# Kernel tuning notes

Hardware: AMD Instinct MI355X
Metric: run time of the kernel (lower is better)

## Reference

```python
import jax, jax.numpy as jnp
import numpy as np
from jax import lax

L, BSZ, H, W, U, P = 16, 8, 32, 32, 128, 256
KB = KC = KD = 3
NUM_GROUPS = 32
DT_MIN, DT_MAX = 1e-3, 1e-1
EPS = 1e-5


def setup_inputs() -> dict:
    key = jax.random.key(0)
    ks = jax.random.split(key, 10)
    return {
        "input_sequence": jax.random.normal(ks[0], (L, BSZ, H, W, U), jnp.float32),
        "x0": jax.random.normal(ks[1], (BSZ, H, W, P), jnp.float32),
        # negative real parts of continuous-time eigenvalues
        "Lambda_re": -(0.5 * jax.random.uniform(ks[2], (P,), jnp.float32) + 1e-2),
        "Lambda_im": jax.random.normal(ks[3], (P,), jnp.float32) * jnp.pi,
        # B param (P,U,kB,kB,2) real/imag stacked (he-normal scale)
        "B_ri": jax.random.normal(ks[4], (P, U, KB, KB, 2), jnp.float32) / np.sqrt(U * KB * KB),
        # C param (U,P,kC,kC,2) real/imag stacked
        "C_ri": jax.random.normal(ks[5], (U, P, KC, KC, 2), jnp.float32) / np.sqrt(P * KC * KC),
        "log_step": jax.random.uniform(ks[6], (P,), jnp.float32) * (np.log(DT_MAX) - np.log(DT_MIN)) + np.log(DT_MIN),
        # diagonal (depthwise) feedthrough D conv kernel, HWIO with I=1
        "D_kernel": jax.random.normal(ks[7], (KD, KD, 1, U), jnp.float32) / KD,
        "gn_scale": jnp.ones((U,), jnp.float32),
        "gn_bias": jnp.zeros((U,), jnp.float32),
    }


def _conv(x, k):
    # x: (N,H,W,Cin), k: (kh,kw,Cin,Cout), SAME padding, stride 1
    return lax.conv_general_dilated(x, k, (1, 1), 'SAME',
                                    dimension_numbers=('NHWC', 'HWIO', 'NHWC'))


def _group_norm(x, scale, bias):
    n, h, w, c = x.shape
    xg = x.reshape(n, h, w, NUM_GROUPS, c // NUM_GROUPS)
    mu = xg.mean(axis=(1, 2, 4), keepdims=True)
    var = xg.var(axis=(1, 2, 4), keepdims=True)
    xg = (xg - mu) * lax.rsqrt(var + EPS)
    return xg.reshape(n, h, w, c) * scale + bias


def reference(input_sequence, x0, Lambda_re, Lambda_im, B_ri, C_ri, log_step,
              D_kernel, gn_scale, gn_bias):
    # ---- discretization (faithful to source discretize_zoh: A_bar = Lambda*Delta, B_bar = Delta*B_tilde) ----
    Lam = jnp.minimum(Lambda_re, -1e-4) + 1j * Lambda_im      # clip_eigs, (P,) complex64
    step = jnp.exp(log_step)                                   # (P,)
    A_bar = Lam * step                                         # (P,) complex64
    # B_bar = (1/Lambda)*Lambda_bar*B_tilde = Delta * B_tilde, laid out HWIO (kB,kB,U,P)
    Bk_r = jnp.transpose(B_ri[..., 0] * step[:, None, None, None], (2, 3, 1, 0))
    Bk_i = jnp.transpose(B_ri[..., 1] * step[:, None, None, None], (2, 3, 1, 0))
    # C_tilde kernel HWIO (kC,kC,P,U)
    Ck_r = jnp.transpose(C_ri[..., 0], (2, 3, 1, 0))
    Ck_i = jnp.transpose(C_ri[..., 1], (2, 3, 1, 0))

    # ---- B (*) u for all timesteps (fold L into batch) ----
    u = input_sequence.reshape(L * BSZ, H, W, U)
    Bus = (_conv(u, Bk_r) + 1j * _conv(u, Bk_i)).reshape(L, BSZ, H, W, P)  # complex64
    Bus = Bus.at[0].add(A_bar * x0.astype(Bus.dtype))

    # ---- diagonal parallel scan: x_k = A * x_{k-1} + (B (*) u_k) ----
    A_elems = jnp.broadcast_to(A_bar[None, None, None, None, :], (L, 1, 1, 1, P))

    def binop(qi, qj):
        Ai, bi = qi
        Aj, bj = qj
        return Aj * Ai, Aj * bi + bj

    _, xs = lax.associative_scan(binop, (A_elems, Bus))        # xs: (L,BSZ,H,W,P) complex

    # ---- ys = 2*Re(C (*) x) ----
    xr = xs.real.reshape(L * BSZ, H, W, P)
    xi = xs.imag.reshape(L * BSZ, H, W, P)
    ys = 2.0 * (_conv(xr, Ck_r) - _conv(xi, Ck_i))             # (L*BSZ,H,W,U)

    # ---- C_D conv head ('standard' Diag_CD_Conv): diagonal D feedthrough + GroupNorm + act ----
    Du = lax.conv_general_dilated(u, D_kernel, (1, 1), 'SAME',
                                  dimension_numbers=('NHWC', 'HWIO', 'NHWC'),
                                  feature_group_count=U)
    h = jax.nn.gelu(_group_norm(ys + Du, gn_scale, gn_bias))
    ys_out = h.reshape(L, BSZ, H, W, U)

    x_last = xs[-1]                                            # (BSZ,H,W,P) complex
    x_last_ri = jnp.stack([x_last.real, x_last.imag], axis=-1) # real view for harness
    return x_last_ri, ys_out
```

## Files before the change

### kernel.cpp

```cpp
#include <hip/hip_runtime.h>
#include <hip/hip_bf16.h>
#include <math.h>

#define Ldim 16
#define BATCH 8
#define HWdim 1024

typedef __attribute__((ext_vector_type(8))) short s8v;
typedef __attribute__((ext_vector_type(4))) short s4v;
typedef __attribute__((ext_vector_type(2))) short s2v;
typedef __attribute__((ext_vector_type(4))) float f32x4;
typedef __attribute__((ext_vector_type(2))) float f32x2;

__device__ __forceinline__ short f2bf(float f) {
    __hip_bfloat16 h = __float2bfloat16(f);
    return __builtin_bit_cast(short, h);
}
__device__ __forceinline__ float bf2f(short s) {
    __hip_bfloat16 h = __builtin_bit_cast(__hip_bfloat16, s);
    return __bfloat162float(h);
}

__device__ __forceinline__ void gload_lds16(const short* g, short* l) {
    __builtin_amdgcn_global_load_lds(
        (const __attribute__((address_space(1))) void*)g,
        (__attribute__((address_space(3))) void*)l, 16, 0, 0);
}

__global__ __launch_bounds__(256)
void prep_kernel(const float* __restrict__ Lre, const float* __restrict__ Lim,
                 const float* __restrict__ B_ri, const float* __restrict__ C_ri,
                 const float* __restrict__ log_step, short* __restrict__ Wb,
                 short* __restrict__ Wc, float* __restrict__ Abar) {
    int tid = blockIdx.x * 256 + threadIdx.x;
    if (tid < 256) {
        float st = expf(log_step[tid]);
        Abar[tid] = fminf(Lre[tid], -1e-4f) * st;
        Abar[256 + tid] = Lim[tid] * st;
    }
    const int total = 9 * 512 * 128;
    for (int i = tid; i < total; i += gridDim.x * 256) {
        int tile = i >> 13;
        int r = i & 8191;
        int A = r * 2;
        int cout_lc = A >> 7;
        int remb = A & 127;
        int ci2 = remb ^ ((cout_lc & 7) << 4);
        int ci_local = ci2 >> 1;
        {
            int cgp = tile / 18;
            int rm = tile % 18;
            int ch = rm / 9, t = rm % 9;
            int cout = cgp * 128 + cout_lc;
            int p = cout >> 1, ri = cout & 1;
            int u = ch * 64 + ci_local;
            float val = B_ri[(((size_t)p * 128 + u) * 9 + t) * 2 + ri] * expf(log_step[p]);
            Wb[i] = f2bf(val);
        }
        {
            int ch = tile / 9;
            int t = tile % 9;
            int u = cout_lc;
            int k = ch * 64 + ci_local;
            int p = k >> 1, ri = k & 1;
            float val = C_ri[(((size_t)u * 256 + p) * 9 + t) * 2 + ri];
            val = ri ? -2.f * val : 2.f * val;
            Wc[i] = f2bf(val);
        }
    }
}

__global__ __launch_bounds__(256)
void ubf_kernel(const float* __restrict__ u, short* __restrict__ Ubf) {
    size_t t8 = ((size_t)blockIdx.x * 256 + threadIdx.x) * 8;
    f32x4 v0 = *(const f32x4*)(u + t8);
    f32x4 v1 = *(const f32x4*)(u + t8 + 4);
    s8v o;
#pragma unroll
    for (int j = 0; j < 4; ++j) { o[j] = f2bf(v0[j]); o[4 + j] = f2bf(v1[j]); }
    *(s8v*)(Ubf + t8) = o;
}

template <int CIN, int COUT, bool INF32, bool INFULL, bool RMW>
__global__ __launch_bounds__(256, 2)
void conv_mfma(const void* __restrict__ inbuf, const short* __restrict__ Wt,
               short* __restrict__ outbuf, int b0, int Gshift) {
    constexpr int NCH = CIN / 64;
    constexpr int NT = NCH * 9;
    __shared__ short ilds[6 * 34 * 64];
    __shared__ short wlds[3 * 8192];

    const int tid = threadIdx.x;
    const int lane = tid & 63;
    const int wv = tid >> 6;
    const int waveM = wv & 1, waveN = wv >> 1;
    const int lm = lane & 15, quad = lane >> 4;
    const int h0 = blockIdx.x * 4;
    const int cgp = blockIdx.y;
    const int img = blockIdx.z;
    const int l = img >> Gshift;
    const int bi = img & ((1 << Gshift) - 1);
    const size_t inframe = INFULL ? (size_t)(l * BATCH + b0 + bi) : (size_t)img;

    constexpr int NST = 7;
    uint goff[NST];
    int laddr[NST];
#pragma unroll
    for (int j = 0; j < NST; ++j) {
        int idx = tid + j * 256;
        laddr[j] = -1;
        goff[j] = 0xFFFFFFFFu;
        if (idx < 6 * 34 * 8) {
            int cgi = idx & 7;
            int pos = idx >> 3;
            int w34 = pos % 34;
            int sr = pos / 34;
            int habs = h0 - 1 + sr, wabs = w34 - 1;
            laddr[j] = ((pos << 3) + (cgi ^ (pos & 7))) << 3;
            if ((unsigned)habs < 32u && (unsigned)wabs < 32u)
                goff[j] = (uint)(((uint)inframe * HWdim + habs * 32 + wabs) * CIN + cgi * 8);
        }
    }

    auto issue_W = [&](int j) {
        const short* src = Wt + ((size_t)cgp * NT + j) * 8192;
        short* dst = &wlds[(j % 3) * 8192];
#pragma unroll
        for (int r = 0; r < 4; ++r)
            gload_lds16(src + (size_t)(r * 256 + tid) * 8, dst + (r * 256 + wv * 64) * 8);
    };

    auto stage_input = [&](int ch) {
        s8v sreg[NST];
#pragma unroll
        for (int j = 0; j < NST; ++j) {
            s8v v = (s8v){0, 0, 0, 0, 0, 0, 0, 0};
            if (goff[j] != 0xFFFFFFFFu) {
                if constexpr (INF32) {
                    const float* src = (const float*)inbuf + goff[j] + ch * 64;
                    f32x4 a0 = *(const f32x4*)src;
                    f32x4 a1 = *(const f32x4*)(src + 4);
#pragma unroll
                    for (int q = 0; q < 4; ++q) { v[q] = f2bf(a0[q]); v[4 + q] = f2bf(a1[q]); }
                } else {
                    v = *(const s8v*)((const short*)inbuf + goff[j] + ch * 64);
                }
            }
            sreg[j] = v;
        }
#pragma unroll
        for (int j = 0; j < NST; ++j)
            if (laddr[j] >= 0) *(s8v*)&ilds[laddr[j]] = sreg[j];
    };

    f32x4 acc[4][4];
#pragma unroll
    for (int mt = 0; mt < 4; ++mt)
#pragma unroll
        for (int nt = 0; nt < 4; ++nt)
            acc[mt][nt] = (f32x4){0.f, 0.f, 0.f, 0.f};

    auto compute_tap = [&](int t, const short* wb) {
        int kh = t / 3, kw = t - kh * 3;
#pragma unroll
        for (int ks = 0; ks < 2; ++ks) {
            s8v a[4], b[4];
#pragma unroll
            for (int mt = 0; mt < 4; ++mt) {
                int p = (waveM * 2 + (mt >> 1) + kh) * 34 + (mt & 1) * 16 + lm + kw;
                int c = ks * 4 + quad;
                a[mt] = *(const s8v*)&ilds[(((p << 3) + (c ^ (p & 7))) << 3)];
            }
#pragma unroll
            for (int nt = 0; nt < 4; ++nt) {
                int cl = waveN * 64 + nt * 16 + lm;
                int ba = (cl * 128 + ks * 64 + quad * 16) ^ ((cl & 7) << 4);
                b[nt] = *(const s8v*)((const char*)wb + ba);
            }
            __builtin_amdgcn_s_setprio(1);
#pragma unroll
            for (int mt = 0; mt < 4; ++mt)
#pragma unroll
                for (int nt = 0; nt < 4; ++nt)
                    acc[mt][nt] = __builtin_amdgcn_mfma_f32_16x16x32_bf16(
                        a[mt], b[nt], acc[mt][nt], 0, 0, 0);
            __builtin_amdgcn_s_setprio(0);
        }
    };

    issue_W(0);
    if (NT > 1) issue_W(1);
    stage_input(0);
    asm volatile("s_waitcnt vmcnt(0) lgkmcnt(0)" ::: "memory");
    __builtin_amdgcn_sched_barrier(0);
    __builtin_amdgcn_s_barrier();

#pragma unroll
    for (int k = 0; k < NT; ++k) {
        const int ch = k / 9;
        const int t = k - ch * 9;
        if (k + 2 < NT) issue_W(k + 2);
        compute_tap(t, &wlds[(k % 3) * 8192]);
        if (k + 1 < NT) {
            if (k + 2 < NT) {
                asm volatile("s_waitcnt vmcnt(4)" ::: "memory");
            } else {
                asm volatile("s_waitcnt vmcnt(0)" ::: "memory");
            }
            __builtin_amdgcn_sched_barrier(0);
            __builtin_amdgcn_s_barrier();
            if (t == 8) {
                stage_input(ch + 1);
                asm volatile("s_waitcnt lgkmcnt(0)" ::: "memory");
                __builtin_amdgcn_sched_barrier(0);
                __builtin_amdgcn_s_barrier();
            }
        }
    }

#pragma unroll
    for (int mt = 0; mt < 4; ++mt) {
#pragma unroll
        for (int reg = 0; reg < 4; ++reg) {
            int mm = waveM * 64 + mt * 16 + quad * 4 + reg;
            int r = mm >> 5, w = mm & 31;
            size_t rowbase = ((size_t)img * HWdim + (h0 + r) * 32 + w) * COUT +
                             cgp * 128 + waveN * 64 + lm;
#pragma unroll
            for (int nt = 0; nt < 4; ++nt) {
                size_t oidx = rowbase + nt * 16;
                float val = acc[mt][nt][reg];
                if (RMW) val += bf2f(outbuf[oidx]);
                outbuf[oidx] = f2bf(val);
            }
        }
    }
}

__global__ __launch_bounds__(256)
void scan_kernel(const float* __restrict__ x0, const float* __restrict__ Abar,
                 short* __restrict__ X, float* __restrict__ out_xlast, int b0, int G) {
    int p = threadIdx.x;
    int hw = blockIdx.x;
    int bi = blockIdx.y;
    int b = b0 + bi;
    float Ar = Abar[p], Ai = Abar[256 + p];
    float xr = x0[((size_t)b * HWdim + hw) * 256 + p];
    float xi = 0.f;
    for (int l = 0; l < Ldim; ++l) {
        size_t base = ((size_t)(l * G + bi) * HWdim + hw) * 512 + p * 2;
        s2v v = *(s2v*)&X[base];
        float br = bf2f(v[0]), bim = bf2f(v[1]);
        float nr = Ar * xr - Ai * xi + br;
        float ni = Ar * xi + Ai * xr + bim;
        xr = nr; xi = ni;
        v[0] = f2bf(xr); v[1] = f2bf(xi);
        *(s2v*)&X[base] = v;
    }
    f32x2 o2 = {xr, xi};
    *(f32x2*)&out_xlast[(((size_t)b * HWdim + hw) * 256 + p) * 2] = o2;
}

template <bool UBF>
__global__ __launch_bounds__(256)
void du_kernel(const void* __restrict__ uin, const float* __restrict__ Dk,
               short* __restrict__ ys, int b0, int Gshift) {
    int tid = blockIdx.x * 256 + threadIdx.x;
    int c4 = tid & 31;
    int hw = (tid >> 5) & 1023;
    int img = tid >> 15;
    int h = hw >> 5, w = hw & 31;
    int l = img >> Gshift, bi = img & ((1 << Gshift) - 1);
    size_t fbase = ((size_t)(l * BATCH + b0 + bi)) * HWdim * 128;
    float s0 = 0.f, s1 = 0.f, s2 = 0.f, s3 = 0.f;
#pragma unroll
    for (int kh = 0; kh < 3; ++kh)
#pragma unroll
        for (int kw = 0; kw < 3; ++kw) {
            int hh = h + kh - 1, wc = w + kw - 1;
            if ((unsigned)hh < 32u && (unsigned)wc < 32u) {
                f32x4 d = *(const f32x4*)&Dk[(kh * 3 + kw) * 128 + c4 * 4];
                size_t off = fbase + ((size_t)hh * 32 + wc) * 128 + c4 * 4;
                if (UBF) {
                    s4v v = *(const s4v*)((const short*)uin + off);
                    s0 += bf2f(v[0]) * d[0]; s1 += bf2f(v[1]) * d[1];
                    s2 += bf2f(v[2]) * d[2]; s3 += bf2f(v[3]) * d[3];
                } else {
                    f32x4 v = *(const f32x4*)((const float*)uin + off);
                    s0 += v[0] * d[0]; s1 += v[1] * d[1];
                    s2 += v[2] * d[2]; s3 += v[3] * d[3];
                }
            }
        }
    s4v o = {f2bf(s0), f2bf(s1), f2bf(s2), f2bf(s3)};
    *(s4v*)&ys[(size_t)tid * 4] = o;
}

__global__ __launch_bounds__(256)
void gnstats_kernel(const short* __restrict__ ys, float* __restrict__ stats) {
    int g = blockIdx.x;
    int img = blockIdx.y;
    int tid = threadIdx.x;
    float s = 0.f, s2 = 0.f;
    for (int hw = tid; hw < HWdim; hw += 256) {
        s4v v = *(const s4v*)&ys[((size_t)img * HWdim + hw) * 128 + g * 4];
#pragma unroll
        for (int j = 0; j < 4; ++j) {
            float f = bf2f(v[j]);
            s += f; s2 += f * f;
        }
    }
    __shared__ float red[16];
    for (int off = 32; off > 0; off >>= 1) {
        s += __shfl_down(s, off, 64);
        s2 += __shfl_down(s2, off, 64);
    }
    int wid = tid >> 6;
    if ((tid & 63) == 0) { red[wid] = s; red[8 + wid] = s2; }
    __syncthreads();
    if (tid == 0) {
        float S = 0.f, S2 = 0.f;
        for (int w2 = 0; w2 < 4; ++w2) { S += red[w2]; S2 += red[8 + w2]; }
        const float inv = 1.f / (HWdim * 4);
        float mean = S * inv;
        float var = S2 * inv - mean * mean;
        stats[(img * 32 + g) * 2 + 0] = mean;
        stats[(img * 32 + g) * 2 + 1] = var;
    }
}

__global__ __launch_bounds__(256)
void gnapply_kernel(const short* __restrict__ ys, const float* __restrict__ stats,
                    const float* __restrict__ scale, const float* __restrict__ bias,
                    float* __restrict__ out_ys, int b0, int Gshift) {
    int tid = blockIdx.x * 256 + threadIdx.x;
    int c4 = tid & 31;
    int hw = (tid >> 5) & 1023;
    int img = tid >> 15;
    int l = img >> Gshift, bi = img & ((1 << Gshift) - 1);
    float mean = stats[(img * 32 + c4) * 2 + 0];
    float var = stats[(img * 32 + c4) * 2 + 1];
    float rstd = rsqrtf(var + 1e-5f);
    s4v v = *(const s4v*)&ys[(size_t)tid * 4];
    f32x4 sc = *(const f32x4*)&scale[c4 * 4];
    f32x4 bs = *(const f32x4*)&bias[c4 * 4];
    f32x4 o;
    const float kAlpha = 0.7978845608028654f;
#pragma unroll
    for (int j = 0; j < 4; ++j) {
        float y = (bf2f(v[j]) - mean) * rstd * sc[j] + bs[j];
        float t = kAlpha * (y + 0.044715f * y * y * y);
        o[j] = 0.5f * y * (1.f + tanhf(t));
    }
    *(f32x4*)&out_ys[(((size_t)(l * BATCH + b0 + bi)) * HWdim + hw) * 128 + c4 * 4] = o;
}

extern "C" void kernel_launch(void* const* d_in, const int* in_sizes, int n_in,
                              void* d_out, int out_size, void* d_ws, size_t ws_size,
                              hipStream_t stream) {
    const float* useq = (const float*)d_in[0];
    const float* x0 = (const float*)d_in[1];
    const float* Lre = (const float*)d_in[2];
    const float* Lim = (const float*)d_in[3];
    const float* B_ri = (const float*)d_in[4];
    const float* C_ri = (const float*)d_in[5];
    const float* log_step = (const float*)d_in[6];
    const float* Dk = (const float*)d_in[7];
    const float* gsc = (const float*)d_in[8];
    const float* gbi = (const float*)d_in[9];
    float* out = (float*)d_out;

    const size_t WBYTES = 9 * 512 * 128 * 2;
    const size_t UBF_BYTES = (size_t)Ldim * BATCH * HWdim * 128 * 2;

    int G = 2;
    bool ubf = false;
    {
        auto need = [&](int g, bool u) -> size_t {
            size_t base = 2 * WBYTES + 2048 + (size_t)g * 4096;
            size_t x = (size_t)g * Ldim * HWdim * 512 * 2;
            size_t ysb = (size_t)g * Ldim * HWdim * 128 * 2;
            return base + x + ysb + (u ? UBF_BYTES : 0);
        };
        if (ws_size >= need(8, true)) { G = 8; ubf = true; }
        else if (ws_size >= need(8, false)) { G = 8; }
        else if (ws_size >= need(4, true)) { G = 4; ubf = true; }
        else if (ws_size >= need(4, false)) { G = 4; }
        else if (ws_size >= need(2, true)) { G = 2; ubf = true; }
    }
    int Gshift = (G == 8) ? 3 : (G == 4) ? 2 : 1;
    int imgs = Ldim * G;

    char* wsb = (char*)d_ws;
    short* Wb = (short*)(wsb);
    short* Wc = (short*)(wsb + WBYTES);
    float* Abar = (float*)(wsb + 2 * WBYTES);
    float* stats = (float*)(wsb + 2 * WBYTES + 2048);
    size_t offX = 2 * WBYTES + 2048 + (size_t)G * 4096;
    short* X = (short*)(wsb + offX);
    size_t offYS = offX + (size_t)G * Ldim * HWdim * 512 * 2;
    short* YS = (short*)(wsb + offYS);
    short* Ubf = (short*)(wsb + offYS + (size_t)G * Ldim * HWdim * 128 * 2);

    prep_kernel<<<2304, 256, 0, stream>>>(Lre, Lim, B_ri, C_ri, log_step, Wb, Wc, Abar);
    if (ubf) ubf_kernel<<<8192, 256, 0, stream>>>(useq, Ubf);

    for (int b0 = 0; b0 < BATCH; b0 += G) {
        if (ubf)
            conv_mfma<128, 512, false, true, false><<<dim3(8, 4, imgs), 256, 0, stream>>>(
                Ubf, Wb, X, b0, Gshift);
        else
            conv_mfma<128, 512, true, true, false><<<dim3(8, 4, imgs), 256, 0, stream>>>(
                useq, Wb, X, b0, Gshift);
        scan_kernel<<<dim3(HWdim, G), 256, 0, stream>>>(x0, Abar, X, out, b0, G);
        if (ubf)
            du_kernel<true><<<imgs * 128, 256, 0, stream>>>(Ubf, Dk, YS, b0, Gshift);
        else
            du_kernel<false><<<imgs * 128, 256, 0, stream>>>(useq, Dk, YS, b0, Gshift);
        conv_mfma<512, 128, false, false, true><<<dim3(8, 1, imgs), 256, 0, stream>>>(
            X, Wc, YS, b0, Gshift);
        gnstats_kernel<<<dim3(32, imgs), 256, 0, stream>>>(YS, stats);
        gnapply_kernel<<<imgs * 128, 256, 0, stream>>>(YS, stats, gsc, gbi, out + 4194304, b0,
                                                       Gshift);
    }
}
```

Measured before the change: 585.9 us.

## Swizzle conv workgroups across XCDs, vectorize epilogue stores, slice bf16 input per group

The 3D conv grids become 1D grids whose block index is remapped so that consecutive workgroups landing on the same XCD share an image and weight tiles, which is meant to improve L2 locality. The MFMA operands are swapped so each lane holds four consecutive output channels, allowing 8-byte vector stores and RMW loads in the epilogue instead of scalar bf16 accesses. The bf16 input conversion is now done per batch group into a smaller buffer, which reduces the workspace needed so the ubf path fits more often, at the cost of one extra launch per group.

```diff
diff --git a/kernel.cpp b/kernel.cpp
--- a/kernel.cpp
+++ b/kernel.cpp
@@ -71,14 +71,20 @@
 }
 
 __global__ __launch_bounds__(256)
-void ubf_kernel(const float* __restrict__ u, short* __restrict__ Ubf) {
-    size_t t8 = ((size_t)blockIdx.x * 256 + threadIdx.x) * 8;
-    f32x4 v0 = *(const f32x4*)(u + t8);
-    f32x4 v1 = *(const f32x4*)(u + t8 + 4);
+void ubf_slice_kernel(const float* __restrict__ u, short* __restrict__ Ubf,
+                      int b0, int Gshift) {
+    size_t t = (size_t)blockIdx.x * 256 + threadIdx.x;
+    int c8 = (int)(t & 15);
+    int hw = (int)(t >> 4) & 1023;
+    int img = (int)(t >> 14);
+    int l = img >> Gshift, bi = img & ((1 << Gshift) - 1);
+    const float* src = u + (((size_t)(l * BATCH + b0 + bi) * HWdim + hw) * 128 + c8 * 8);
+    f32x4 v0 = *(const f32x4*)src;
+    f32x4 v1 = *(const f32x4*)(src + 4);
     s8v o;
 #pragma unroll
     for (int j = 0; j < 4; ++j) { o[j] = f2bf(v0[j]); o[4 + j] = f2bf(v1[j]); }
-    *(s8v*)(Ubf + t8) = o;
+    *(s8v*)(Ubf + ((size_t)img * HWdim + hw) * 128 + c8 * 8) = o;
 }
 
 template <int CIN, int COUT, bool INF32, bool INFULL, bool RMW>
@@ -87,6 +93,7 @@
                short* __restrict__ outbuf, int b0, int Gshift) {
     constexpr int NCH = CIN / 64;
     constexpr int NT = NCH * 9;
+    constexpr int NCGP = COUT / 128;
     __shared__ short ilds[6 * 34 * 64];
     __shared__ short wlds[3 * 8192];
 
@@ -95,9 +102,14 @@
     const int wv = tid >> 6;
     const int waveM = wv & 1, waveN = wv >> 1;
     const int lm = lane & 15, quad = lane >> 4;
-    const int h0 = blockIdx.x * 4;
-    const int cgp = blockIdx.y;
-    const int img = blockIdx.z;
+
+    const int chunk = gridDim.x >> 3;
+    const int wg = blockIdx.x;
+    const int wgs = (wg & 7) * chunk + (wg >> 3);
+    const int cgp = wgs % NCGP;
+    const int h0 = (((wgs / NCGP) & 7)) * 4;
+    const int img = wgs / (NCGP * 8);
+
     const int l = img >> Gshift;
     const int bi = img & ((1 << Gshift) - 1);
     const size_t inframe = INFULL ? (size_t)(l * BATCH + b0 + bi) : (size_t)img;
@@ -183,7 +195,7 @@
 #pragma unroll
                 for (int nt = 0; nt < 4; ++nt)
                     acc[mt][nt] = __builtin_amdgcn_mfma_f32_16x16x32_bf16(
-                        a[mt], b[nt], acc[mt][nt], 0, 0, 0);
+                        b[nt], a[mt], acc[mt][nt], 0, 0, 0);
             __builtin_amdgcn_s_setprio(0);
         }
     };
@@ -220,19 +232,25 @@
 
 #pragma unroll
     for (int mt = 0; mt < 4; ++mt) {
-#pragma unroll
-        for (int reg = 0; reg < 4; ++reg) {
-            int mm = waveM * 64 + mt * 16 + quad * 4 + reg;
-            int r = mm >> 5, w = mm & 31;
-            size_t rowbase = ((size_t)img * HWdim + (h0 + r) * 32 + w) * COUT +
-                             cgp * 128 + waveN * 64 + lm;
-#pragma unroll
-            for (int nt = 0; nt < 4; ++nt) {
-                size_t oidx = rowbase + nt * 16;
-                float val = acc[mt][nt][reg];
-                if (RMW) val += bf2f(outbuf[oidx]);
-                outbuf[oidx] = f2bf(val);
-            }
+        int px = waveM * 64 + mt * 16 + lm;
+        int r = px >> 5, w = px & 31;
+        size_t rowbase = ((size_t)img * HWdim + (h0 + r) * 32 + w) * COUT +
+                         cgp * 128 + waveN * 64 + quad * 4;
+#pragma unroll
+        for (int nt = 0; nt < 4; ++nt) {
+            size_t oidx = rowbase + nt * 16;
+            s4v o;
+            if (RMW) {
+                s4v old = *(const s4v*)&outbuf[oidx];
+#pragma unroll
+                for (int reg = 0; reg < 4; ++reg)
+                    o[reg] = f2bf(acc[mt][nt][reg] + bf2f(old[reg]));
+            } else {
+#pragma unroll
+                for (int reg = 0; reg < 4; ++reg)
+                    o[reg] = f2bf(acc[mt][nt][reg]);
+            }
+            *(s4v*)&outbuf[oidx] = o;
         }
     }
 }
@@ -271,7 +289,8 @@
     int img = tid >> 15;
     int h = hw >> 5, w = hw & 31;
     int l = img >> Gshift, bi = img & ((1 << Gshift) - 1);
-    size_t fbase = ((size_t)(l * BATCH + b0 + bi)) * HWdim * 128;
+    size_t fbase = UBF ? (size_t)img * HWdim * 128
+                       : ((size_t)(l * BATCH + b0 + bi)) * HWdim * 128;
     float s0 = 0.f, s1 = 0.f, s2 = 0.f, s3 = 0.f;
 #pragma unroll
     for (int kh = 0; kh < 3; ++kh)
@@ -371,7 +390,6 @@
     float* out = (float*)d_out;
 
     const size_t WBYTES = 9 * 512 * 128 * 2;
-    const size_t UBF_BYTES = (size_t)Ldim * BATCH * HWdim * 128 * 2;
 
     int G = 2;
     bool ubf = false;
@@ -380,7 +398,8 @@
             size_t base = 2 * WBYTES + 2048 + (size_t)g * 4096;
             size_t x = (size_t)g * Ldim * HWdim * 512 * 2;
             size_t ysb = (size_t)g * Ldim * HWdim * 128 * 2;
-            return base + x + ysb + (u ? UBF_BYTES : 0);
+            size_t ub = (size_t)g * Ldim * HWdim * 128 * 2;
+            return base + x + ysb + (u ? ub : 0);
         };
         if (ws_size >= need(8, true)) { G = 8; ubf = true; }
         else if (ws_size >= need(8, false)) { G = 8; }
@@ -403,21 +422,22 @@
     short* Ubf = (short*)(wsb + offYS + (size_t)G * Ldim * HWdim * 128 * 2);
 
     prep_kernel<<<2304, 256, 0, stream>>>(Lre, Lim, B_ri, C_ri, log_step, Wb, Wc, Abar);
-    if (ubf) ubf_kernel<<<8192, 256, 0, stream>>>(useq, Ubf);
 
     for (int b0 = 0; b0 < BATCH; b0 += G) {
-        if (ubf)
-            conv_mfma<128, 512, false, true, false><<<dim3(8, 4, imgs), 256, 0, stream>>>(
+        if (ubf) {
+            ubf_slice_kernel<<<imgs * 64, 256, 0, stream>>>(useq, Ubf, b0, Gshift);
+            conv_mfma<128, 512, false, false, false><<<8 * 4 * imgs, 256, 0, stream>>>(
                 Ubf, Wb, X, b0, Gshift);
-        else
-            conv_mfma<128, 512, true, true, false><<<dim3(8, 4, imgs), 256, 0, stream>>>(
+        } else {
+            conv_mfma<128, 512, true, true, false><<<8 * 4 * imgs, 256, 0, stream>>>(
                 useq, Wb, X, b0, Gshift);
+        }
         scan_kernel<<<dim3(HWdim, G), 256, 0, stream>>>(x0, Abar, X, out, b0, G);
         if (ubf)
             du_kernel<true><<<imgs * 128, 256, 0, stream>>>(Ubf, Dk, YS, b0, Gshift);
         else
             du_kernel<false><<<imgs * 128, 256, 0, stream>>>(useq, Dk, YS, b0, Gshift);
-        conv_mfma<512, 128, false, false, true><<<dim3(8, 1, imgs), 256, 0, stream>>>(
+        conv_mfma<512, 128, false, false, true><<<8 * imgs, 256, 0, stream>>>(
             X, Wc, YS, b0, Gshift);
         gnstats_kernel<<<dim3(32, imgs), 256, 0, stream>>>(YS, stats);
         gnapply_kernel<<<imgs * 128, 256, 0, stream>>>(YS, stats, gsc, gbi, out + 4194304, b0,
```

Measured after the change: 609.6 us. 1.04x slower.

## Prefetch next input chunk across MFMA taps and batch scan loads per thread

Applied to the files above, without the earlier changes.

In the conv kernel's bf16-input path, the next channel chunk's global loads are issued before the last tap's MFMAs and written to LDS after the barrier, so global latency overlaps compute instead of stalling at chunk boundaries. The scan kernel now has each thread handle two channels with vector loads, hoists all 16 timestep loads ahead of the recurrence, and stores x_last with a nontemporal write. The prefetch keeps extra registers live during compute, which may lower occupancy, and the scan launches half as many blocks.

```diff
diff --git a/kernel.cpp b/kernel.cpp
--- a/kernel.cpp
+++ b/kernel.cpp
@@ -130,6 +130,21 @@
             gload_lds16(src + (size_t)(r * 256 + tid) * 8, dst + (r * 256 + wv * 64) * 8);
     };
 
+    auto stage_load = [&](int ch, s8v* sreg) {
+#pragma unroll
+        for (int j = 0; j < NST; ++j) {
+            s8v v = (s8v){0, 0, 0, 0, 0, 0, 0, 0};
+            if (goff[j] != 0xFFFFFFFFu)
+                v = *(const s8v*)((const short*)inbuf + goff[j] + ch * 64);
+            sreg[j] = v;
+        }
+    };
+    auto stage_write = [&](const s8v* sreg) {
+#pragma unroll
+        for (int j = 0; j < NST; ++j)
+            if (laddr[j] >= 0) *(s8v*)&ilds[laddr[j]] = sreg[j];
+    };
+
     auto stage_input = [&](int ch) {
         s8v sreg[NST];
 #pragma unroll
@@ -199,8 +214,16 @@
     for (int k = 0; k < NT; ++k) {
         const int ch = k / 9;
         const int t = k - ch * 9;
+        const bool boundary = (t == 8) && (k + 1 < NT);
+
+        s8v sreg[NST];
+        if (boundary && !INF32) {
+            stage_load(ch + 1, sreg);
+            __builtin_amdgcn_sched_barrier(0);
+        }
         if (k + 2 < NT) issue_W(k + 2);
         compute_tap(t, &wlds[(k % 3) * 8192]);
+
         if (k + 1 < NT) {
             if (k + 2 < NT) {
                 asm volatile("s_waitcnt vmcnt(4)" ::: "memory");
@@ -209,8 +232,12 @@
             }
             __builtin_amdgcn_sched_barrier(0);
             __builtin_amdgcn_s_barrier();
-            if (t == 8) {
-                stage_input(ch + 1);
+            if (boundary) {
+                if (!INF32) {
+                    stage_write(sreg);
+                } else {
+                    stage_input(ch + 1);
+                }
                 asm volatile("s_waitcnt lgkmcnt(0)" ::: "memory");
                 __builtin_amdgcn_sched_barrier(0);
                 __builtin_amdgcn_s_barrier();
@@ -240,25 +267,39 @@
 __global__ __launch_bounds__(256)
 void scan_kernel(const float* __restrict__ x0, const float* __restrict__ Abar,
                  short* __restrict__ X, float* __restrict__ out_xlast, int b0, int G) {
-    int p = threadIdx.x;
-    int hw = blockIdx.x;
+    int tid = threadIdx.x;
+    int pp = tid & 127;
+    int sub = tid >> 7;
+    int hw = blockIdx.x * 2 + sub;
     int bi = blockIdx.y;
     int b = b0 + bi;
-    float Ar = Abar[p], Ai = Abar[256 + p];
-    float xr = x0[((size_t)b * HWdim + hw) * 256 + p];
-    float xi = 0.f;
+    int p0 = pp * 2;
+    float Ar0 = Abar[p0], Ar1 = Abar[p0 + 1];
+    float Ai0 = Abar[256 + p0], Ai1 = Abar[256 + p0 + 1];
+    f32x2 x0v = *(const f32x2*)&x0[((size_t)b * HWdim + hw) * 256 + p0];
+    float xr0 = x0v[0], xi0 = 0.f;
+    float xr1 = x0v[1], xi1 = 0.f;
+
+    s4v v[Ldim];
+#pragma unroll
+    for (int l = 0; l < Ldim; ++l)
+        v[l] = *(const s4v*)&X[((size_t)(l * G + bi) * HWdim + hw) * 512 + pp * 4];
+
+#pragma unroll
     for (int l = 0; l < Ldim; ++l) {
-        size_t base = ((size_t)(l * G + bi) * HWdim + hw) * 512 + p * 2;
-        s2v v = *(s2v*)&X[base];
-        float br = bf2f(v[0]), bim = bf2f(v[1]);
-        float nr = Ar * xr - Ai * xi + br;
-        float ni = Ar * xi + Ai * xr + bim;
-        xr = nr; xi = ni;
-        v[0] = f2bf(xr); v[1] = f2bf(xi);
-        *(s2v*)&X[base] = v;
-    }
-    f32x2 o2 = {xr, xi};
-    *(f32x2*)&out_xlast[(((size_t)b * HWdim + hw) * 256 + p) * 2] = o2;
+        float br0 = bf2f(v[l][0]), bm0 = bf2f(v[l][1]);
+        float br1 = bf2f(v[l][2]), bm1 = bf2f(v[l][3]);
+        float nr0 = Ar0 * xr0 - Ai0 * xi0 + br0;
+        float ni0 = Ar0 * xi0 + Ai0 * xr0 + bm0;
+        float nr1 = Ar1 * xr1 - Ai1 * xi1 + br1;
+        float ni1 = Ar1 * xi1 + Ai1 * xr1 + bm1;
+        xr0 = nr0; xi0 = ni0; xr1 = nr1; xi1 = ni1;
+        s4v o = {f2bf(xr0), f2bf(xi0), f2bf(xr1), f2bf(xi1)};
+        *(s4v*)&X[((size_t)(l * G + bi) * HWdim + hw) * 512 + pp * 4] = o;
+    }
+    f32x4 ox = {xr0, xi0, xr1, xi1};
+    __builtin_nontemporal_store(
+        ox, (f32x4*)&out_xlast[(((size_t)b * HWdim + hw) * 256 + p0) * 2]);
 }
 
 template <bool UBF>
@@ -412,7 +453,7 @@
         else
             conv_mfma<128, 512, true, true, false><<<dim3(8, 4, imgs), 256, 0, stream>>>(
                 useq, Wb, X, b0, Gshift);
-        scan_kernel<<<dim3(HWdim, G), 256, 0, stream>>>(x0, Abar, X, out, b0, G);
+        scan_kernel<<<dim3(HWdim / 2, G), 256, 0, stream>>>(x0, Abar, X, out, b0, G);
         if (ubf)
             du_kernel<true><<<imgs * 128, 256, 0, stream>>>(Ubf, Dk, YS, b0, Gshift);
         else
```

New measurement: 599.9 us. +2.4%, slower.
